# Optimization experiments

Measured on AMD Instinct MI355X. Metric: run time of the kernel, lower is better.

The kernel has to match this reference:

```python
import jax, jax.numpy as jnp
import numpy as np

NUM_HEADS = 8
WS = 7          # window size (hardcoded in source)
SR = 4          # sr_ratio
EPS = 1e-5


def _win_partition(t, ws, H, W):
    # t: [B, h, N, d] -> [B*h*nW, ws*ws, d]
    B, h, N, d = t.shape
    t = t.reshape(B * h, H // ws, ws, W // ws, ws, d)
    t = t.transpose(0, 1, 3, 2, 4, 5)
    return t.reshape(-1, ws * ws, d)


def _win_reverse(w, ws, H, W, h):
    # w: [B*h*nW, ws*ws, d] -> [B, H*W, h*d]
    d = w.shape[-1]
    Bh = w.shape[0] // ((H // ws) * (W // ws))
    x = w.reshape(Bh, H // ws, W // ws, ws, ws, d).transpose(0, 1, 3, 2, 4, 5)
    x = x.reshape(Bh // h, h, H, W, d).transpose(0, 2, 3, 1, 4)
    return x.reshape(Bh // h, H * W, h * d)


def setup_inputs() -> dict:
    key = jax.random.key(0)
    B, H, W, C = 32, 56, 56, 256
    N = H * W
    ks = jax.random.split(key, 10)
    s = lambda k, shp: jax.random.normal(k, shp, dtype=jnp.float32) * 0.02
    return {
        "x": jax.random.normal(ks[0], (B, N, C), dtype=jnp.float32),
        "lepe_lin_w": s(ks[1], (C, C)), "lepe_lin_b": jnp.zeros((C,), jnp.float32),
        "lepe_conv_w": s(ks[2], (3, 3, 1, C)), "lepe_conv_b": jnp.zeros((C,), jnp.float32),
        "sr_w": s(ks[3], (SR, SR, C, C)), "sr_b": jnp.zeros((C,), jnp.float32),
        "norm_g": jnp.ones((C,), jnp.float32), "norm_b": jnp.zeros((C,), jnp.float32),
        "q1_w": s(ks[4], (C, C // 2)), "kv1_w": s(ks[5], (C, C)),
        "q2_w": s(ks[6], (C, C // 2)), "kv2_w": s(ks[7], (C, C)),
        "proj_w": s(ks[8], (C, C)), "proj_b": jnp.zeros((C,), jnp.float32),
        "H": H, "W": W,
    }


def reference(x, lepe_lin_w, lepe_lin_b, lepe_conv_w, lepe_conv_b, sr_w, sr_b,
              norm_g, norm_b, q1_w, kv1_w, q2_w, kv2_w, proj_w, proj_b, H, W):
    B, N, C = x.shape
    h2 = NUM_HEADS // 2
    d = C // NUM_HEADS
    scale = d ** (-0.5)

    # lepe: linear -> depthwise 3x3 conv (NHWC) -> flatten back
    lep = (x @ lepe_lin_w + lepe_lin_b).reshape(B, H, W, C)
    lep = jax.lax.conv_general_dilated(
        lep, lepe_conv_w, window_strides=(1, 1), padding='SAME',
        dimension_numbers=('NHWC', 'HWIO', 'NHWC'), feature_group_count=C) + lepe_conv_b
    lepe = lep.reshape(B, N, C)

    # --- branch 1: global attention over sr-downsampled kv ---
    q1 = (x @ q1_w).reshape(B, N, h2, d).transpose(0, 2, 1, 3)         # [B,h2,N,d]
    img = x.reshape(B, H, W, C)
    x1_ = jax.lax.conv_general_dilated(
        img, sr_w, window_strides=(SR, SR), padding='VALID',
        dimension_numbers=('NHWC', 'HWIO', 'NHWC')) + sr_b              # [B,H/sr,W/sr,C]
    x1_ = x1_.reshape(B, -1, C)                                         # [B,N1,C]
    mu = jnp.mean(x1_, axis=-1, keepdims=True)
    var = jnp.mean(jnp.square(x1_ - mu), axis=-1, keepdims=True)
    x1_ = (x1_ - mu) * jax.lax.rsqrt(var + EPS) * norm_g + norm_b
    x1_ = jax.nn.gelu(x1_, approximate=False)
    kv1 = (x1_ @ kv1_w).reshape(B, -1, 2, h2, d).transpose(2, 0, 3, 1, 4)
    k1, v1 = kv1[0], kv1[1]                                             # [B,h2,N1,d]
    attn1 = jax.nn.softmax(jnp.einsum('bhnd,bhmd->bhnm', q1, k1) * scale, axis=-1)
    x1 = jnp.einsum('bhnm,bhmd->bhnd', attn1, v1)
    x1 = x1.transpose(0, 2, 1, 3).reshape(B, N, C // 2)

    # --- branch 2: 7x7 window attention ---
    q2 = (x @ q2_w).reshape(B, N, h2, d).transpose(0, 2, 1, 3)          # [B,h2,N,d]
    kv2 = (x @ kv2_w).reshape(B, -1, 2, h2, d).transpose(2, 0, 3, 1, 4)
    k2, v2 = kv2[0], kv2[1]
    q2w = _win_partition(q2, WS, H, W)                                  # [B*h2*nW,49,d]
    k2w = _win_partition(k2, WS, H, W)
    v2w = _win_partition(v2, WS, H, W)
    attn2 = jax.nn.softmax(jnp.einsum('wnd,wmd->wnm', q2w, k2w) * scale, axis=-1)
    x2w = jnp.einsum('wnm,wmd->wnd', attn2, v2w)
    x2 = _win_reverse(x2w, WS, H, W, h2)                                # [B,N,C/2]

    out = jnp.concatenate([x1, x2], axis=-1)
    out = (out + lepe) @ proj_w + proj_b
    return out
```

## Files before the change

kernel.cpp:

```cpp
#include <hip/hip_runtime.h>
#include <hip/hip_bf16.h>

typedef __hip_bfloat16 bf16;
typedef __attribute__((ext_vector_type(8))) short short8;
typedef __attribute__((ext_vector_type(4))) float floatx4;

__device__ __forceinline__ float toF(bf16 v){ return __bfloat162float(v); }
__device__ __forceinline__ float b2f(unsigned short u){
  return __uint_as_float(((unsigned int)u) << 16);
}
__device__ __forceinline__ unsigned short f2bu(float f){
  bf16 h = __float2bfloat16(f);
  return *(unsigned short*)&h;
}

__global__ __launch_bounds__(256) void prep_all_kernel(
    const float* __restrict__ x, bf16* __restrict__ xb,
    const float* __restrict__ sr_w, const float* __restrict__ lepe_w,
    const float* __restrict__ kv2_w, const float* __restrict__ q1_w,
    const float* __restrict__ q2_w, const float* __restrict__ kv1_w,
    const float* __restrict__ proj_w,
    bf16* __restrict__ wT_sr, bf16* __restrict__ wT_x,
    bf16* __restrict__ wT_kv1, bf16* __restrict__ wT_proj,
    int* __restrict__ srbase) {
  const int tid = threadIdx.x;
  if (blockIdx.x < 25088) {
    size_t i4 = ((size_t)blockIdx.x * 256 + tid) * 4;
    float4 v = *(const float4*)(x + i4);
    ushort4 o;
    o.x = f2bu(v.x); o.y = f2bu(v.y); o.z = f2bu(v.z); o.w = f2bu(v.w);
    *(ushort4*)(xb + i4) = o;
    return;
  }
  const int bid = blockIdx.x - 25088;
  const float* src; bf16* dst; int K, N, idx;
  if (bid < 4096)      { src = sr_w;   dst = wT_sr;          K = 4096; N = 256; idx = bid * 256 + tid; }
  else if (bid < 4352) { src = lepe_w; dst = wT_x;           K = 256;  N = 256; idx = (bid - 4096) * 256 + tid; }
  else if (bid < 4608) { src = kv2_w;  dst = wT_x + 65536;   K = 256;  N = 256; idx = (bid - 4352) * 256 + tid; }
  else if (bid < 4736) { src = q1_w;   dst = wT_x + 131072;  K = 256;  N = 128; idx = (bid - 4608) * 256 + tid; }
  else if (bid < 4864) { src = q2_w;   dst = wT_x + 163840;  K = 256;  N = 128; idx = (bid - 4736) * 256 + tid; }
  else if (bid < 5120) { src = kv1_w;  dst = wT_kv1;         K = 256;  N = 256; idx = (bid - 4864) * 256 + tid; }
  else if (bid < 5376) { src = proj_w; dst = wT_proj;        K = 256;  N = 256; idx = (bid - 5120) * 256 + tid; }
  else {
    int t = (bid - 5376) * 256 + tid;
    if (t < 6272) {
      int b = t / 196, p = t - b * 196;
      int oy = p / 14, ox = p - oy * 14;
      srbase[t] = ((b * 56 + oy * 4) * 56 + ox * 4) * 256;
    }
    return;
  }
  int k = idx / N, n = idx - k * N;
  dst[(size_t)n * K + k] = __float2bfloat16(src[idx]);
}

__global__ __launch_bounds__(256) void gemm_x3(
    const bf16* __restrict__ A, const bf16* __restrict__ BT,
    const float* __restrict__ lepe_b,
    bf16* __restrict__ L1, bf16* __restrict__ KV2, bf16* __restrict__ Q12) {
  __shared__ uint4 As[128 * 5];
  __shared__ uint4 Bs[128 * 5];
  const int sw = (blockIdx.x & 7) * 588 + (blockIdx.x >> 3);
  const int bx = sw % 6, by = sw / 6;
  const int m0 = by * 128;
  const int n0 = bx * 128;
  const int tid = threadIdx.x;
  const int wave = tid >> 6, lane = tid & 63;
  const int wm = (wave >> 1) * 64, wn = (wave & 1) * 64;
  const int l15 = lane & 15, quad = lane >> 4;
  const int row0 = tid >> 2, row1 = 64 + (tid >> 2), seg = tid & 3;
  const bf16* aP0 = A + (size_t)(m0 + row0) * 256 + seg * 8;
  const bf16* aP1 = A + (size_t)(m0 + row1) * 256 + seg * 8;
  const bf16* bP0 = BT + (size_t)(n0 + row0) * 256 + seg * 8;
  const bf16* bP1 = BT + (size_t)(n0 + row1) * 256 + seg * 8;
  floatx4 zero = {0.f, 0.f, 0.f, 0.f};
  floatx4 acc[4][4];
#pragma unroll
  for (int i = 0; i < 4; i++)
#pragma unroll
    for (int j = 0; j < 4; j++) acc[i][j] = zero;

  uint4 a0 = *(const uint4*)aP0, a1 = *(const uint4*)aP1;
  uint4 b0 = *(const uint4*)bP0, b1 = *(const uint4*)bP1;
#pragma unroll
  for (int t = 0; t < 8; t++) {
    As[row0 * 5 + seg] = a0; As[row1 * 5 + seg] = a1;
    Bs[row0 * 5 + seg] = b0; Bs[row1 * 5 + seg] = b1;
    __syncthreads();
    if (t < 7) {
      int k0 = (t + 1) * 32;
      a0 = *(const uint4*)(aP0 + k0); a1 = *(const uint4*)(aP1 + k0);
      b0 = *(const uint4*)(bP0 + k0); b1 = *(const uint4*)(bP1 + k0);
    }
    short8 af[4], bfr[4];
#pragma unroll
    for (int i = 0; i < 4; i++)
      af[i] = *(const short8*)&As[(wm + i * 16 + l15) * 5 + quad];
#pragma unroll
    for (int j = 0; j < 4; j++)
      bfr[j] = *(const short8*)&Bs[(wn + j * 16 + l15) * 5 + quad];
#pragma unroll
    for (int i = 0; i < 4; i++)
#pragma unroll
      for (int j = 0; j < 4; j++)
        acc[i][j] = __builtin_amdgcn_mfma_f32_16x16x32_bf16(bfr[j], af[i], acc[i][j], 0, 0, 0);
    __syncthreads();
  }
  const int segN = n0 >> 8;
  bf16* Cd = (segN == 0) ? L1 : (segN == 1) ? KV2 : Q12;
  const int nc0 = n0 & 255;
#pragma unroll
  for (int i = 0; i < 4; i++) {
    int m = m0 + wm + i * 16 + l15;
#pragma unroll
    for (int j = 0; j < 4; j++) {
      int nb = nc0 + wn + j * 16 + quad * 4;
      float4 bv = {0.f, 0.f, 0.f, 0.f};
      if (segN == 0) bv = *(const float4*)&lepe_b[nb];
      ushort4 o;
      o.x = f2bu(acc[i][j][0] + bv.x);
      o.y = f2bu(acc[i][j][1] + bv.y);
      o.z = f2bu(acc[i][j][2] + bv.z);
      o.w = f2bu(acc[i][j][3] + bv.w);
      *(ushort4*)&Cd[(size_t)m * 256 + nb] = o;
    }
  }
}

__global__ __launch_bounds__(256) void gemm_sr(
    const bf16* __restrict__ X, const bf16* __restrict__ BT,
    const int* __restrict__ base, float* __restrict__ C) {
  __shared__ uint4 As[128 * 5];
  __shared__ uint4 Bs[128 * 5];
  const int tid = threadIdx.x;
  const int m0 = blockIdx.y * 128;
  const int n0 = blockIdx.x * 128;
  const int kz = blockIdx.z;
  const int wave = tid >> 6, lane = tid & 63;
  const int wm = (wave >> 1) * 64, wn = (wave & 1) * 64;
  const int l15 = lane & 15, quad = lane >> 4;
  const int row0 = tid >> 2, row1 = 64 + (tid >> 2), seg = tid & 3;
  const int mb0 = base[m0 + row0];
  const int mb1 = base[m0 + row1];
  const bf16* bP0 = BT + (size_t)(n0 + row0) * 4096 + seg * 8;
  const bf16* bP1 = BT + (size_t)(n0 + row1) * 4096 + seg * 8;
  const int kbeg = kz * 512;
  floatx4 zero = {0.f, 0.f, 0.f, 0.f};
  floatx4 acc[4][4];
#pragma unroll
  for (int i = 0; i < 4; i++)
#pragma unroll
    for (int j = 0; j < 4; j++) acc[i][j] = zero;

  uint4 a0, a1, b0, b1;
  {
    int k = kbeg + seg * 8;
    int kp = k >> 8, c = k & 255;
    int off = ((kp >> 2) * 56 + (kp & 3)) * 256 + c;
    a0 = *(const uint4*)(X + (size_t)mb0 + off);
    a1 = *(const uint4*)(X + (size_t)mb1 + off);
    b0 = *(const uint4*)(bP0 + kbeg);
    b1 = *(const uint4*)(bP1 + kbeg);
  }
  for (int t = 0; t < 16; t++) {
    As[row0 * 5 + seg] = a0; As[row1 * 5 + seg] = a1;
    Bs[row0 * 5 + seg] = b0; Bs[row1 * 5 + seg] = b1;
    __syncthreads();
    if (t < 15) {
      int k = kbeg + (t + 1) * 32 + seg * 8;
      int kp = k >> 8, c = k & 255;
      int off = ((kp >> 2) * 56 + (kp & 3)) * 256 + c;
      a0 = *(const uint4*)(X + (size_t)mb0 + off);
      a1 = *(const uint4*)(X + (size_t)mb1 + off);
      b0 = *(const uint4*)(bP0 + kbeg + (t + 1) * 32);
      b1 = *(const uint4*)(bP1 + kbeg + (t + 1) * 32);
    }
    short8 af[4], bfr[4];
#pragma unroll
    for (int i = 0; i < 4; i++)
      af[i] = *(const short8*)&As[(wm + i * 16 + l15) * 5 + quad];
#pragma unroll
    for (int j = 0; j < 4; j++)
      bfr[j] = *(const short8*)&Bs[(wn + j * 16 + l15) * 5 + quad];
#pragma unroll
    for (int i = 0; i < 4; i++)
#pragma unroll
      for (int j = 0; j < 4; j++)
        acc[i][j] = __builtin_amdgcn_mfma_f32_16x16x32_bf16(bfr[j], af[i], acc[i][j], 0, 0, 0);
    __syncthreads();
  }
  float* Cp = C + (size_t)kz * (6272 * 256);
#pragma unroll
  for (int i = 0; i < 4; i++) {
    int m = m0 + wm + i * 16 + l15;
#pragma unroll
    for (int j = 0; j < 4; j++) {
      int nb = n0 + wn + j * 16 + quad * 4;
      float4 o = {acc[i][j][0], acc[i][j][1], acc[i][j][2], acc[i][j][3]};
      *(float4*)&Cp[(size_t)m * 256 + nb] = o;
    }
  }
}

__global__ __launch_bounds__(256) void gemm_kv1(
    const bf16* __restrict__ A, const bf16* __restrict__ BT,
    bf16* __restrict__ C) {
  __shared__ uint4 As[128 * 5];
  __shared__ uint4 Bs[128 * 5];
  const int tid = threadIdx.x;
  const int m0 = blockIdx.y * 128;
  const int n0 = blockIdx.x * 128;
  const int wave = tid >> 6, lane = tid & 63;
  const int wm = (wave >> 1) * 64, wn = (wave & 1) * 64;
  const int l15 = lane & 15, quad = lane >> 4;
  const int row0 = tid >> 2, row1 = 64 + (tid >> 2), seg = tid & 3;
  const bf16* aP0 = A + (size_t)(m0 + row0) * 256 + seg * 8;
  const bf16* aP1 = A + (size_t)(m0 + row1) * 256 + seg * 8;
  const bf16* bP0 = BT + (size_t)(n0 + row0) * 256 + seg * 8;
  const bf16* bP1 = BT + (size_t)(n0 + row1) * 256 + seg * 8;
  floatx4 zero = {0.f, 0.f, 0.f, 0.f};
  floatx4 acc[4][4];
#pragma unroll
  for (int i = 0; i < 4; i++)
#pragma unroll
    for (int j = 0; j < 4; j++) acc[i][j] = zero;

  uint4 a0 = *(const uint4*)aP0, a1 = *(const uint4*)aP1;
  uint4 b0 = *(const uint4*)bP0, b1 = *(const uint4*)bP1;
#pragma unroll
  for (int t = 0; t < 8; t++) {
    As[row0 * 5 + seg] = a0; As[row1 * 5 + seg] = a1;
    Bs[row0 * 5 + seg] = b0; Bs[row1 * 5 + seg] = b1;
    __syncthreads();
    if (t < 7) {
      int k0 = (t + 1) * 32;
      a0 = *(const uint4*)(aP0 + k0); a1 = *(const uint4*)(aP1 + k0);
      b0 = *(const uint4*)(bP0 + k0); b1 = *(const uint4*)(bP1 + k0);
    }
    short8 af[4], bfr[4];
#pragma unroll
    for (int i = 0; i < 4; i++)
      af[i] = *(const short8*)&As[(wm + i * 16 + l15) * 5 + quad];
#pragma unroll
    for (int j = 0; j < 4; j++)
      bfr[j] = *(const short8*)&Bs[(wn + j * 16 + l15) * 5 + quad];
#pragma unroll
    for (int i = 0; i < 4; i++)
#pragma unroll
      for (int j = 0; j < 4; j++)
        acc[i][j] = __builtin_amdgcn_mfma_f32_16x16x32_bf16(bfr[j], af[i], acc[i][j], 0, 0, 0);
    __syncthreads();
  }
#pragma unroll
  for (int i = 0; i < 4; i++) {
    int m = m0 + wm + i * 16 + l15;
#pragma unroll
    for (int j = 0; j < 4; j++) {
      int nb = n0 + wn + j * 16 + quad * 4;
      ushort4 o;
      o.x = f2bu(acc[i][j][0]); o.y = f2bu(acc[i][j][1]);
      o.z = f2bu(acc[i][j][2]); o.w = f2bu(acc[i][j][3]);
      *(ushort4*)&C[(size_t)m * 256 + nb] = o;
    }
  }
}

__global__ __launch_bounds__(256) void gemm_proj_mfma(
    const bf16* __restrict__ X1, const bf16* __restrict__ X2,
    const bf16* __restrict__ L2, const bf16* __restrict__ BT,
    const float* __restrict__ bias, float* __restrict__ C) {
  __shared__ uint4 As[128 * 5];
  __shared__ uint4 Bs[128 * 5];
  const int sw = (blockIdx.x & 7) * 196 + (blockIdx.x >> 3);
  const int tid = threadIdx.x;
  const int m0 = (sw >> 1) * 128;
  const int n0 = (sw & 1) * 128;
  const int wave = tid >> 6, lane = tid & 63;
  const int wm = (wave >> 1) * 64, wn = (wave & 1) * 64;
  const int l15 = lane & 15, quad = lane >> 4;
  const int row0 = tid >> 2, row1 = 64 + (tid >> 2), seg = tid & 3;
  const bf16* bP0 = BT + (size_t)(n0 + row0) * 256 + seg * 8;
  const bf16* bP1 = BT + (size_t)(n0 + row1) * 256 + seg * 8;
  floatx4 zero = {0.f, 0.f, 0.f, 0.f};
  floatx4 acc[4][4];
#pragma unroll
  for (int i = 0; i < 4; i++)
#pragma unroll
    for (int j = 0; j < 4; j++) acc[i][j] = zero;

  uint4 va0, va1, vl0, vl1, b0, b1;
  {
    int k = seg * 8;
    const bf16* s0 = X1 + (size_t)(m0 + row0) * 128 + k;
    const bf16* s1 = X1 + (size_t)(m0 + row1) * 128 + k;
    va0 = *(const uint4*)s0; va1 = *(const uint4*)s1;
    vl0 = *(const uint4*)(L2 + (size_t)(m0 + row0) * 256 + k);
    vl1 = *(const uint4*)(L2 + (size_t)(m0 + row1) * 256 + k);
    b0 = *(const uint4*)bP0; b1 = *(const uint4*)bP1;
  }
#pragma unroll
  for (int t = 0; t < 8; t++) {
    {
      unsigned short o0[8], o1[8];
      const unsigned short* pa0 = (const unsigned short*)&va0;
      const unsigned short* pl0 = (const unsigned short*)&vl0;
      const unsigned short* pa1 = (const unsigned short*)&va1;
      const unsigned short* pl1 = (const unsigned short*)&vl1;
#pragma unroll
      for (int e = 0; e < 8; e++) {
        o0[e] = f2bu(b2f(pa0[e]) + b2f(pl0[e]));
        o1[e] = f2bu(b2f(pa1[e]) + b2f(pl1[e]));
      }
      As[row0 * 5 + seg] = *(const uint4*)o0;
      As[row1 * 5 + seg] = *(const uint4*)o1;
      Bs[row0 * 5 + seg] = b0;
      Bs[row1 * 5 + seg] = b1;
    }
    __syncthreads();
    if (t < 7) {
      int k = (t + 1) * 32 + seg * 8;
      const bf16* s0 = (k < 128) ? X1 + (size_t)(m0 + row0) * 128 + k
                                 : X2 + (size_t)(m0 + row0) * 128 + (k - 128);
      const bf16* s1 = (k < 128) ? X1 + (size_t)(m0 + row1) * 128 + k
                                 : X2 + (size_t)(m0 + row1) * 128 + (k - 128);
      va0 = *(const uint4*)s0; va1 = *(const uint4*)s1;
      vl0 = *(const uint4*)(L2 + (size_t)(m0 + row0) * 256 + k);
      vl1 = *(const uint4*)(L2 + (size_t)(m0 + row1) * 256 + k);
      b0 = *(const uint4*)(bP0 + (t + 1) * 32);
      b1 = *(const uint4*)(bP1 + (t + 1) * 32);
    }
    short8 af[4], bfr[4];
#pragma unroll
    for (int i = 0; i < 4; i++)
      af[i] = *(const short8*)&As[(wm + i * 16 + l15) * 5 + quad];
#pragma unroll
    for (int j = 0; j < 4; j++)
      bfr[j] = *(const short8*)&Bs[(wn + j * 16 + l15) * 5 + quad];
#pragma unroll
    for (int i = 0; i < 4; i++)
#pragma unroll
      for (int j = 0; j < 4; j++)
        acc[i][j] = __builtin_amdgcn_mfma_f32_16x16x32_bf16(bfr[j], af[i], acc[i][j], 0, 0, 0);
    __syncthreads();
  }
#pragma unroll
  for (int i = 0; i < 4; i++) {
    int m = m0 + wm + i * 16 + l15;
#pragma unroll
    for (int j = 0; j < 4; j++) {
      int nb = n0 + wn + j * 16 + quad * 4;
      float4 bv = *(const float4*)&bias[nb];
      float4 o = {acc[i][j][0] + bv.x, acc[i][j][1] + bv.y,
                  acc[i][j][2] + bv.z, acc[i][j][3] + bv.w};
      *(float4*)&C[(size_t)m * 256 + nb] = o;
    }
  }
}

__global__ __launch_bounds__(256) void dwconv8_kernel(
    const bf16* __restrict__ in, const float* __restrict__ w,
    const float* __restrict__ bias, bf16* __restrict__ out) {
  const int idx = blockIdx.x * 256 + threadIdx.x;
  const int c8 = (idx & 31) * 8;
  const int sp = idx >> 5;
  const int xx = sp % 56;
  const int yb = sp / 56;
  const int yy = yb % 56;
  const int b  = yb / 56;
  float4 bb0 = *(const float4*)&bias[c8];
  float4 bb1 = *(const float4*)&bias[c8 + 4];
  float acc[8] = {bb0.x, bb0.y, bb0.z, bb0.w, bb1.x, bb1.y, bb1.z, bb1.w};
#pragma unroll
  for (int dy = 0; dy < 3; dy++) {
    int y = yy + dy - 1;
    if ((unsigned)y >= 56u) continue;
#pragma unroll
    for (int dx = 0; dx < 3; dx++) {
      int x = xx + dx - 1;
      if ((unsigned)x >= 56u) continue;
      uint4 v = *(const uint4*)&in[((size_t)((b * 56 + y) * 56 + x)) * 256 + c8];
      const unsigned short* pv = (const unsigned short*)&v;
      float4 w0 = *(const float4*)&w[(dy * 3 + dx) * 256 + c8];
      float4 w1 = *(const float4*)&w[(dy * 3 + dx) * 256 + c8 + 4];
      float wf[8] = {w0.x, w0.y, w0.z, w0.w, w1.x, w1.y, w1.z, w1.w};
#pragma unroll
      for (int e = 0; e < 8; e++) acc[e] += b2f(pv[e]) * wf[e];
    }
  }
  unsigned short o[8];
#pragma unroll
  for (int e = 0; e < 8; e++) o[e] = f2bu(acc[e]);
  *(uint4*)&out[(size_t)sp * 256 + c8] = *(const uint4*)o;
}

__global__ __launch_bounds__(256) void ln_gelu_kernel(
    const float* __restrict__ in, const float* __restrict__ srb,
    const float* __restrict__ g, const float* __restrict__ bb,
    bf16* __restrict__ out) {
  const int tok = blockIdx.x;
  const int tid = threadIdx.x;
  float v = srb[tid];
  const float* p = in + (size_t)tok * 256 + tid;
#pragma unroll
  for (int c = 0; c < 8; c++) v += p[(size_t)c * 1605632];
  float s = v, s2 = v * v;
#pragma unroll
  for (int o = 32; o > 0; o >>= 1) {
    s += __shfl_down(s, o, 64);
    s2 += __shfl_down(s2, o, 64);
  }
  __shared__ float rs[4], rs2[4];
  int wid = tid >> 6, lane = tid & 63;
  if (lane == 0) { rs[wid] = s; rs2[wid] = s2; }
  __syncthreads();
  float tot = rs[0] + rs[1] + rs[2] + rs[3];
  float tot2 = rs2[0] + rs2[1] + rs2[2] + rs2[3];
  float mean = tot * (1.0f / 256.0f);
  float var = tot2 * (1.0f / 256.0f) - mean * mean;
  float y = (v - mean) * rsqrtf(var + 1e-5f) * g[tid] + bb[tid];
  out[(size_t)tok * 256 + tid] =
      __float2bfloat16(0.5f * y * (1.0f + erff(y * 0.70710678118654752f)));
}

__global__ __launch_bounds__(256) void attn1_mfma(
    const bf16* __restrict__ Q12, const bf16* __restrict__ KV,
    bf16* __restrict__ O) {
  __shared__ bf16 sk[224 * 32];
  __shared__ bf16 svT[32 * 232];
  __shared__ bf16 pbuf[4][64 * 32];
  const int b = blockIdx.z, h = blockIdx.y, chunk = blockIdx.x;
  const int tid = threadIdx.x;
  const int wave = tid >> 6, lane = tid & 63;
  const int l15 = lane & 15, quad = lane >> 4;
  for (int i = tid; i < 224 * 4; i += 256) {
    int m = i >> 2, c = i & 3;
    uint4 kv4 = {0u, 0u, 0u, 0u}, vv4 = {0u, 0u, 0u, 0u};
    if (m < 196) {
      const bf16* p = KV + ((size_t)(b * 196 + m)) * 256 + h * 32 + c * 8;
      kv4 = *(const uint4*)p;
      vv4 = *(const uint4*)(p + 128);
    }
    *(uint4*)&sk[m * 32 + c * 8] = kv4;
    const unsigned short* pv = (const unsigned short*)&vv4;
#pragma unroll
    for (int e = 0; e < 8; e++)
      *(unsigned short*)&svT[(c * 8 + e) * 232 + m] = pv[e];
  }
  __syncthreads();
  const int q0 = chunk * 256 + wave * 64;
  short8 aq[4];
#pragma unroll
  for (int i = 0; i < 4; i++) {
    int qr = q0 + i * 16 + l15; if (qr > 3135) qr = 3135;
    aq[i] = *(const short8*)(Q12 + ((size_t)(b * 3136 + qr)) * 256 + h * 32 + quad * 8);
  }
  const float scale = 0.17677669529663687f;
  floatx4 zero = {0.f, 0.f, 0.f, 0.f};
  floatx4 acc[4][2];
  float lsum[4][4];
#pragma unroll
  for (int i = 0; i < 4; i++) {
    acc[i][0] = zero; acc[i][1] = zero;
#pragma unroll
    for (int r = 0; r < 4; r++) lsum[i][r] = 0.f;
  }
  bf16* pw = pbuf[wave];
  for (int c = 0; c < 7; c++) {
    const int kv0 = c * 32;
    short8 bk[2];
#pragma unroll
    for (int n = 0; n < 2; n++)
      bk[n] = *(const short8*)&sk[(kv0 + n * 16 + l15) * 32 + quad * 8];
    floatx4 s[4][2];
#pragma unroll
    for (int i = 0; i < 4; i++)
#pragma unroll
      for (int n = 0; n < 2; n++)
        s[i][n] = __builtin_amdgcn_mfma_f32_16x16x32_bf16(aq[i], bk[n], zero, 0, 0, 0);
#pragma unroll
    for (int i = 0; i < 4; i++)
#pragma unroll
      for (int n = 0; n < 2; n++) {
        bool valid = (kv0 + n * 16 + l15) < 196;
#pragma unroll
        for (int r = 0; r < 4; r++) {
          float p = valid ? __expf(s[i][n][r] * scale) : 0.f;
          lsum[i][r] += p;
          pw[(i * 16 + quad * 4 + r) * 32 + n * 16 + l15] = __float2bfloat16(p);
        }
      }
    asm volatile("s_waitcnt lgkmcnt(0)" ::: "memory");
    short8 ap[4], bv[2];
#pragma unroll
    for (int i = 0; i < 4; i++)
      ap[i] = *(const short8*)&pw[(i * 16 + l15) * 32 + quad * 8];
#pragma unroll
    for (int n = 0; n < 2; n++)
      bv[n] = *(const short8*)&svT[(n * 16 + l15) * 232 + kv0 + quad * 8];
#pragma unroll
    for (int i = 0; i < 4; i++)
#pragma unroll
      for (int n = 0; n < 2; n++)
        acc[i][n] = __builtin_amdgcn_mfma_f32_16x16x32_bf16(ap[i], bv[n], acc[i][n], 0, 0, 0);
  }
#pragma unroll
  for (int i = 0; i < 4; i++)
#pragma unroll
    for (int r = 0; r < 4; r++) {
      float v = lsum[i][r];
      v += __shfl_xor(v, 1, 64);
      v += __shfl_xor(v, 2, 64);
      v += __shfl_xor(v, 4, 64);
      v += __shfl_xor(v, 8, 64);
      lsum[i][r] = 1.0f / v;
    }
#pragma unroll
  for (int i = 0; i < 4; i++)
#pragma unroll
    for (int r = 0; r < 4; r++) {
      int qr = q0 + i * 16 + quad * 4 + r;
      if (qr < 3136) {
        bf16* op = O + ((size_t)(b * 3136 + qr)) * 128 + h * 32;
        op[l15]      = __float2bfloat16(acc[i][0][r] * lsum[i][r]);
        op[16 + l15] = __float2bfloat16(acc[i][1][r] * lsum[i][r]);
      }
    }
}

__global__ __launch_bounds__(256) void attn2_mfma(
    const bf16* __restrict__ Q12, const bf16* __restrict__ KV2,
    bf16* __restrict__ O) {
  __shared__ bf16 sk[64 * 136];
  __shared__ bf16 pb[4][64 * 72];
  const int b = blockIdx.y;
  const int win = blockIdx.x;
  const int wy = win >> 3, wx = win & 7;
  const int tid = threadIdx.x;
  const int wave = tid >> 6, lane = tid & 63;
  const int l15 = lane & 15, quad = lane >> 4;
  const int h = wave;

  for (int i = tid; i < 49 * 16; i += 256) {
    int m = i >> 4, c = i & 15;
    int iy = m / 7, ix = m - iy * 7;
    int n = (wy * 7 + iy) * 56 + wx * 7 + ix;
    *(uint4*)&sk[m * 136 + c * 8] =
        *(const uint4*)&KV2[((size_t)(b * 3136 + n)) * 256 + c * 8];
  }

  short8 bvv[2][2];
#pragma unroll
  for (int ks = 0; ks < 2; ks++)
#pragma unroll
    for (int nt = 0; nt < 2; nt++)
#pragma unroll
      for (int e = 0; e < 8; e++) {
        int k = ks * 32 + quad * 8 + e; if (k > 48) k = 48;
        int iy = k / 7, ix = k - iy * 7;
        int n = (wy * 7 + iy) * 56 + wx * 7 + ix;
        bvv[ks][nt][e] = ((const short*)KV2)[((size_t)(b * 3136 + n)) * 256
                                             + 128 + h * 32 + nt * 16 + l15];
      }

  short8 aq[4];
#pragma unroll
  for (int i = 0; i < 4; i++) {
    int lq = i * 16 + l15; if (lq > 48) lq = 48;
    int iy = lq / 7, ix = lq - iy * 7;
    int n = (wy * 7 + iy) * 56 + wx * 7 + ix;
    aq[i] = *(const short8*)(Q12 + ((size_t)(b * 3136 + n)) * 256 + 128 + h * 32 + quad * 8);
  }
  __syncthreads();

  const float scale = 0.17677669529663687f;
  floatx4 zero = {0.f, 0.f, 0.f, 0.f};
  floatx4 acc[4][2];
  float lsum[4][4];
#pragma unroll
  for (int i = 0; i < 4; i++) {
    acc[i][0] = zero; acc[i][1] = zero;
#pragma unroll
    for (int r = 0; r < 4; r++) lsum[i][r] = 0.f;
  }
  bf16* pw = pb[wave];
#pragma unroll
  for (int c = 0; c < 2; c++) {
    const int kv0 = c * 32;
    short8 bk[2];
#pragma unroll
    for (int n = 0; n < 2; n++)
      bk[n] = *(const short8*)&sk[(kv0 + n * 16 + l15) * 136 + h * 32 + quad * 8];
    floatx4 s[4][2];
#pragma unroll
    for (int i = 0; i < 4; i++)
#pragma unroll
      for (int n = 0; n < 2; n++)
        s[i][n] = __builtin_amdgcn_mfma_f32_16x16x32_bf16(aq[i], bk[n], zero, 0, 0, 0);
#pragma unroll
    for (int i = 0; i < 4; i++)
#pragma unroll
      for (int n = 0; n < 2; n++) {
        bool valid = (kv0 + n * 16 + l15) < 49;
#pragma unroll
        for (int r = 0; r < 4; r++) {
          float p = valid ? __expf(s[i][n][r] * scale) : 0.f;
          lsum[i][r] += p;
          pw[(i * 16 + quad * 4 + r) * 72 + kv0 + n * 16 + l15] = __float2bfloat16(p);
        }
      }
  }
  asm volatile("s_waitcnt lgkmcnt(0)" ::: "memory");
#pragma unroll
  for (int ks = 0; ks < 2; ks++) {
    short8 ap[4];
#pragma unroll
    for (int i = 0; i < 4; i++)
      ap[i] = *(const short8*)&pw[(i * 16 + l15) * 72 + ks * 32 + quad * 8];
#pragma unroll
    for (int i = 0; i < 4; i++)
#pragma unroll
      for (int nt = 0; nt < 2; nt++)
        acc[i][nt] = __builtin_amdgcn_mfma_f32_16x16x32_bf16(ap[i], bvv[ks][nt], acc[i][nt], 0, 0, 0);
  }
#pragma unroll
  for (int i = 0; i < 4; i++)
#pragma unroll
    for (int r = 0; r < 4; r++) {
      float v = lsum[i][r];
      v += __shfl_xor(v, 1, 64);
      v += __shfl_xor(v, 2, 64);
      v += __shfl_xor(v, 4, 64);
      v += __shfl_xor(v, 8, 64);
      lsum[i][r] = 1.0f / v;
    }
#pragma unroll
  for (int i = 0; i < 4; i++)
#pragma unroll
    for (int r = 0; r < 4; r++) {
      int lq = i * 16 + quad * 4 + r;
      if (lq < 49) {
        int iy = lq / 7, ix = lq - iy * 7;
        int n = (wy * 7 + iy) * 56 + wx * 7 + ix;
        bf16* op = O + ((size_t)(b * 3136 + n)) * 128 + h * 32;
        op[l15]      = __float2bfloat16(acc[i][0][r] * lsum[i][r]);
        op[16 + l15] = __float2bfloat16(acc[i][1][r] * lsum[i][r]);
      }
    }
}

extern "C" void kernel_launch(void* const* d_in, const int* in_sizes, int n_in,
                              void* d_out, int out_size, void* d_ws, size_t ws_size,
                              hipStream_t stream) {
  const float* x           = (const float*)d_in[0];
  const float* lepe_lin_w  = (const float*)d_in[1];
  const float* lepe_lin_b  = (const float*)d_in[2];
  const float* lepe_conv_w = (const float*)d_in[3];
  const float* lepe_conv_b = (const float*)d_in[4];
  const float* sr_w        = (const float*)d_in[5];
  const float* sr_b        = (const float*)d_in[6];
  const float* norm_g      = (const float*)d_in[7];
  const float* norm_b      = (const float*)d_in[8];
  const float* q1_w        = (const float*)d_in[9];
  const float* kv1_w       = (const float*)d_in[10];
  const float* q2_w        = (const float*)d_in[11];
  const float* kv2_w       = (const float*)d_in[12];
  const float* proj_w      = (const float*)d_in[13];
  const float* proj_b      = (const float*)d_in[14];
  float* out = (float*)d_out;

  char* ws = (char*)d_ws;
  char* ob = (char*)d_out;
  const size_t szBNC = 100352ull * 256 * 2;
  const size_t szBNh = 100352ull * 128 * 2;
  bf16*  xb  = (bf16*)ob;
  bf16*  Q12 = (bf16*)(ob + szBNC);
  bf16*  L1  = (bf16*)ws;
  float* X1Ppart = (float*)ws;
  bf16*  X1N = (bf16*)ob;
  bf16*  KV1 = (bf16*)(ob + 8388608);
  bf16*  X1  = (bf16*)ws;
  bf16*  L2  = (bf16*)(ws + szBNC);
  bf16*  X2  = (bf16*)(ws + 2 * szBNC);
  char*  wtb = ws + 2 * szBNC + szBNh;
  bf16* wT_x    = (bf16*)(wtb);
  bf16* wT_kv1  = (bf16*)(wtb + 393216);
  bf16* wT_proj = (bf16*)(wtb + 524288);
  bf16* wT_sr   = (bf16*)(wtb + 655360);
  int*  srbase  = (int*)(wtb + 655360 + 2097152);
  bf16* KV2     = (bf16*)(wtb + 655360 + 2097152 + 32768);

  prep_all_kernel<<<30489, 256, 0, stream>>>(
      x, xb, sr_w, lepe_lin_w, kv2_w, q1_w, q2_w, kv1_w, proj_w,
      wT_sr, wT_x, wT_kv1, wT_proj, srbase);

  gemm_x3<<<4704, 256, 0, stream>>>(xb, wT_x, lepe_lin_b, L1, KV2, Q12);

  dwconv8_kernel<<<12544, 256, 0, stream>>>(L1, lepe_conv_w, lepe_conv_b, L2);

  attn2_mfma<<<dim3(64, 32), 256, 0, stream>>>(Q12, KV2, X2);

  gemm_sr<<<dim3(2, 49, 8), 256, 0, stream>>>(xb, wT_sr, srbase, X1Ppart);
  ln_gelu_kernel<<<6272, 256, 0, stream>>>(X1Ppart, sr_b, norm_g, norm_b, X1N);
  gemm_kv1<<<dim3(2, 49), 256, 0, stream>>>(X1N, wT_kv1, KV1);
  attn1_mfma<<<dim3(13, 4, 32), 256, 0, stream>>>(Q12, KV1, X1);

  gemm_proj_mfma<<<1568, 256, 0, stream>>>(
      X1, X2, L2, wT_proj, proj_b, out);
}
```

Before: 527.8 us.

## Tile weight transposes through shared memory and simplify gemm_x3 loads and epilogue

The weight transpose in the prep kernel now uses 64x64 shared-memory tiles, so both the global reads and the global writes are coalesced. This replaces the scattered per-element strided writes and cuts the transpose block count. gemm_x3 drops its register prefetch of the next K slice and loads each slice directly before the barrier, which removes load/compute overlap. Its MFMA operand order is swapped, and the epilogue now writes scalar bf16 values with column-major lane mapping instead of vectorized ushort4 rows, which may make the output stores less efficient.

Result: no change. 520.6 us (-1.4%).

```diff
diff --git a/kernel.cpp b/kernel.cpp
--- a/kernel.cpp
+++ b/kernel.cpp
@@ -32,26 +32,37 @@
     *(ushort4*)(xb + i4) = o;
     return;
   }
-  const int bid = blockIdx.x - 25088;
-  const float* src; bf16* dst; int K, N, idx;
-  if (bid < 4096)      { src = sr_w;   dst = wT_sr;          K = 4096; N = 256; idx = bid * 256 + tid; }
-  else if (bid < 4352) { src = lepe_w; dst = wT_x;           K = 256;  N = 256; idx = (bid - 4096) * 256 + tid; }
-  else if (bid < 4608) { src = kv2_w;  dst = wT_x + 65536;   K = 256;  N = 256; idx = (bid - 4352) * 256 + tid; }
-  else if (bid < 4736) { src = q1_w;   dst = wT_x + 131072;  K = 256;  N = 128; idx = (bid - 4608) * 256 + tid; }
-  else if (bid < 4864) { src = q2_w;   dst = wT_x + 163840;  K = 256;  N = 128; idx = (bid - 4736) * 256 + tid; }
-  else if (bid < 5120) { src = kv1_w;  dst = wT_kv1;         K = 256;  N = 256; idx = (bid - 4864) * 256 + tid; }
-  else if (bid < 5376) { src = proj_w; dst = wT_proj;        K = 256;  N = 256; idx = (bid - 5120) * 256 + tid; }
+  const int t = blockIdx.x - 25088;
+  __shared__ float s[64][65];
+  const float* src; bf16* dst; int K, N, kt, nt;
+  if (t < 256)      { src = sr_w;   dst = wT_sr;          K = 4096; N = 256; kt = t >> 2;          nt = t & 3; }
+  else if (t < 272) { src = lepe_w; dst = wT_x;           K = 256;  N = 256; kt = (t - 256) >> 2;  nt = (t - 256) & 3; }
+  else if (t < 288) { src = kv2_w;  dst = wT_x + 65536;   K = 256;  N = 256; kt = (t - 272) >> 2;  nt = (t - 272) & 3; }
+  else if (t < 296) { src = q1_w;   dst = wT_x + 131072;  K = 256;  N = 128; kt = (t - 288) >> 1;  nt = (t - 288) & 1; }
+  else if (t < 304) { src = q2_w;   dst = wT_x + 163840;  K = 256;  N = 128; kt = (t - 296) >> 1;  nt = (t - 296) & 1; }
+  else if (t < 320) { src = kv1_w;  dst = wT_kv1;         K = 256;  N = 256; kt = (t - 304) >> 2;  nt = (t - 304) & 3; }
+  else if (t < 336) { src = proj_w; dst = wT_proj;        K = 256;  N = 256; kt = (t - 320) >> 2;  nt = (t - 320) & 3; }
   else {
-    int t = (bid - 5376) * 256 + tid;
-    if (t < 6272) {
-      int b = t / 196, p = t - b * 196;
+    int tt = (t - 336) * 256 + tid;
+    if (tt < 6272) {
+      int b = tt / 196, p = tt - b * 196;
       int oy = p / 14, ox = p - oy * 14;
-      srbase[t] = ((b * 56 + oy * 4) * 56 + ox * 4) * 256;
+      srbase[tt] = ((b * 56 + oy * 4) * 56 + ox * 4) * 256;
     }
     return;
   }
-  int k = idx / N, n = idx - k * N;
-  dst[(size_t)n * K + k] = __float2bfloat16(src[idx]);
+  const int k0 = kt * 64, n0 = nt * 64;
+#pragma unroll
+  for (int p = tid; p < 4096; p += 256) {
+    int k = p >> 6, n = p & 63;
+    s[k][n] = src[(size_t)(k0 + k) * N + n0 + n];
+  }
+  __syncthreads();
+#pragma unroll
+  for (int p = tid; p < 4096; p += 256) {
+    int n = p >> 6, k = p & 63;
+    dst[(size_t)(n0 + n) * K + k0 + k] = __float2bfloat16(s[k][n]);
+  }
 }
 
 __global__ __launch_bounds__(256) void gemm_x3(
@@ -68,11 +79,6 @@
   const int wave = tid >> 6, lane = tid & 63;
   const int wm = (wave >> 1) * 64, wn = (wave & 1) * 64;
   const int l15 = lane & 15, quad = lane >> 4;
-  const int row0 = tid >> 2, row1 = 64 + (tid >> 2), seg = tid & 3;
-  const bf16* aP0 = A + (size_t)(m0 + row0) * 256 + seg * 8;
-  const bf16* aP1 = A + (size_t)(m0 + row1) * 256 + seg * 8;
-  const bf16* bP0 = BT + (size_t)(n0 + row0) * 256 + seg * 8;
-  const bf16* bP1 = BT + (size_t)(n0 + row1) * 256 + seg * 8;
   floatx4 zero = {0.f, 0.f, 0.f, 0.f};
   floatx4 acc[4][4];
 #pragma unroll
@@ -80,18 +86,15 @@
 #pragma unroll
     for (int j = 0; j < 4; j++) acc[i][j] = zero;
 
-  uint4 a0 = *(const uint4*)aP0, a1 = *(const uint4*)aP1;
-  uint4 b0 = *(const uint4*)bP0, b1 = *(const uint4*)bP1;
-#pragma unroll
-  for (int t = 0; t < 8; t++) {
-    As[row0 * 5 + seg] = a0; As[row1 * 5 + seg] = a1;
-    Bs[row0 * 5 + seg] = b0; Bs[row1 * 5 + seg] = b1;
+  for (int k0 = 0; k0 < 256; k0 += 32) {
+#pragma unroll
+    for (int it = 0; it < 2; it++) {
+      int id = it * 256 + tid;
+      int row = id >> 2, seg = id & 3;
+      As[row * 5 + seg] = *(const uint4*)(A + (size_t)(m0 + row) * 256 + k0 + seg * 8);
+      Bs[row * 5 + seg] = *(const uint4*)(BT + (size_t)(n0 + row) * 256 + k0 + seg * 8);
+    }
     __syncthreads();
-    if (t < 7) {
-      int k0 = (t + 1) * 32;
-      a0 = *(const uint4*)(aP0 + k0); a1 = *(const uint4*)(aP1 + k0);
-      b0 = *(const uint4*)(bP0 + k0); b1 = *(const uint4*)(bP1 + k0);
-    }
     short8 af[4], bfr[4];
 #pragma unroll
     for (int i = 0; i < 4; i++)
@@ -103,26 +106,22 @@
     for (int i = 0; i < 4; i++)
 #pragma unroll
       for (int j = 0; j < 4; j++)
-        acc[i][j] = __builtin_amdgcn_mfma_f32_16x16x32_bf16(bfr[j], af[i], acc[i][j], 0, 0, 0);
+        acc[i][j] = __builtin_amdgcn_mfma_f32_16x16x32_bf16(af[i], bfr[j], acc[i][j], 0, 0, 0);
     __syncthreads();
   }
   const int segN = n0 >> 8;
   bf16* Cd = (segN == 0) ? L1 : (segN == 1) ? KV2 : Q12;
   const int nc0 = n0 & 255;
 #pragma unroll
-  for (int i = 0; i < 4; i++) {
-    int m = m0 + wm + i * 16 + l15;
-#pragma unroll
-    for (int j = 0; j < 4; j++) {
-      int nb = nc0 + wn + j * 16 + quad * 4;
-      float4 bv = {0.f, 0.f, 0.f, 0.f};
-      if (segN == 0) bv = *(const float4*)&lepe_b[nb];
-      ushort4 o;
-      o.x = f2bu(acc[i][j][0] + bv.x);
-      o.y = f2bu(acc[i][j][1] + bv.y);
-      o.z = f2bu(acc[i][j][2] + bv.z);
-      o.w = f2bu(acc[i][j][3] + bv.w);
-      *(ushort4*)&Cd[(size_t)m * 256 + nb] = o;
+  for (int j = 0; j < 4; j++) {
+    int nl = nc0 + wn + j * 16 + l15;
+    float bv = (segN == 0) ? lepe_b[nl] : 0.0f;
+#pragma unroll
+    for (int i = 0; i < 4; i++) {
+      int m = m0 + wm + i * 16 + quad * 4;
+#pragma unroll
+      for (int r = 0; r < 4; r++)
+        Cd[(size_t)(m + r) * 256 + nl] = __float2bfloat16(acc[i][j][r] + bv);
     }
   }
 }
@@ -689,7 +688,7 @@
   int*  srbase  = (int*)(wtb + 655360 + 2097152);
   bf16* KV2     = (bf16*)(wtb + 655360 + 2097152 + 32768);
 
-  prep_all_kernel<<<30489, 256, 0, stream>>>(
+  prep_all_kernel<<<25449, 256, 0, stream>>>(
       x, xb, sr_w, lepe_lin_w, kv2_w, q1_w, q2_w, kv1_w, proj_w,
       wT_sr, wT_x, wT_kv1, wT_proj, srbase);
 
```
